# Performance work log

Hardware: AMD Instinct MI355X
Metric: run time of the kernel (lower is better)

## Reference

```python
import jax, jax.numpy as jnp
import numpy as np

MARGIN = 0.2  # init kwarg
_EPS = 1e-12


def _pairwise_dist(x):
    # Euclidean cdist via the Gram trick; safe sqrt so grads stay finite at d=0.
    sq = jnp.sum(x * x, axis=1)
    d2 = sq[:, None] + sq[None, :] - 2.0 * (x @ x.T)
    d2 = jnp.maximum(d2, 0.0)
    safe = jnp.where(d2 > _EPS, d2, _EPS)
    return jnp.where(d2 > _EPS, jnp.sqrt(safe), 0.0)


def setup_inputs() -> dict:
    key = jax.random.key(0)
    k1, k2 = jax.random.split(key)
    B, D = 8192, 128
    embeddings = jax.random.normal(k1, (B, D), dtype=jnp.float32)
    labels = jax.random.randint(k2, (B,), 0, 64)
    return {"embeddings": embeddings, "labels": labels}


def reference(embeddings, labels):
    B = embeddings.shape[0]
    d = _pairwise_dist(embeddings)                      # [B, B]
    eq = labels[None, :] == labels[:, None]             # [B, B] bool (incl. diag)
    pos_mask = eq.astype(d.dtype) - jnp.eye(B, dtype=d.dtype)  # positives, no self
    hardest_positive = jnp.max(d * pos_mask, axis=1)    # [B]
    max_dist = jnp.max(d)
    # push non-negatives (same label, incl. self) out of the min
    hardest_negative = jnp.min(d + max_dist * eq.astype(d.dtype), axis=1)  # [B]
    losses = jax.nn.relu(hardest_positive - hardest_negative + MARGIN)
    return jnp.mean(losses)
```

## Files before the change

kernel.cpp:

```cpp
#include <hip/hip_runtime.h>
#include <hip/hip_bf16.h>


#define BB 8192
#define DD 128
#define MARGIN 0.2f
#define EPS 1e-12f

#define COLS_PER_BLOCK 512
#define STAGE_COLS 64
#define NSTAGES (COLS_PER_BLOCK / STAGE_COLS)
#define STAGE_SHORTS (STAGE_COLS * DD)

typedef __attribute__((ext_vector_type(8))) short short8;
typedef __attribute__((ext_vector_type(4))) float f32x4;

__device__ inline unsigned short f2bf(float f) {
    __hip_bfloat16 h = __float2bfloat16(f);
    unsigned short u;
    __builtin_memcpy(&u, &h, 2);
    return u;
}

__global__ __launch_bounds__(256) void prep_kernel(
    const float* __restrict__ x, const int* __restrict__ lab,
    unsigned short* __restrict__ xb, float2* __restrict__ meta,
    unsigned* __restrict__ hp2, unsigned* __restrict__ mn2) {
    int t = blockIdx.x * blockDim.x + threadIdx.x;
    int row = t >> 5;
    const float4 v = reinterpret_cast<const float4*>(x)[t];

    union { unsigned short u[4]; uint2 w; } p;
    p.u[0] = f2bf(v.x); p.u[1] = f2bf(v.y);
    p.u[2] = f2bf(v.z); p.u[3] = f2bf(v.w);
    reinterpret_cast<uint2*>(xb)[t] = p.w;

    float s = v.x * v.x + v.y * v.y + v.z * v.z + v.w * v.w;
    #pragma unroll
    for (int m = 16; m >= 1; m >>= 1) s += __shfl_xor(s, m, 64);
    if ((t & 31) == 0) meta[row] = make_float2(s, __int_as_float(lab[row]));

    if (t < BB) { hp2[t] = 0u; mn2[t] = 0x7f800000u; }
}

__global__ __launch_bounds__(512, 4) void triplet_main(
    const unsigned short* __restrict__ xb, const float2* __restrict__ meta,
    unsigned* __restrict__ hp2, unsigned* __restrict__ mn2) {
    const int tid  = threadIdx.x;
    const int wave = tid >> 6;
    const int lane = tid & 63;
    const int l15  = lane & 15;
    const int lhi  = lane >> 4;
    const int rbase = blockIdx.x * 128 + wave * 16;
    const int cbase = blockIdx.y * COLS_PER_BLOCK;

    __shared__ unsigned short sb[2][STAGE_SHORTS];
    __shared__ float2 smeta[COLS_PER_BLOCK];

    short8 a[4];
    {
        const unsigned short* ar = xb + (size_t)(rbase + l15) * DD + lhi * 8;
        #pragma unroll
        for (int s = 0; s < 4; ++s)
            a[s] = *reinterpret_cast<const short8*>(ar + s * 32);
    }
    float sqi[4]; int li[4]; float hp[4], mn[4];
    #pragma unroll
    for (int r = 0; r < 4; ++r) {
        float2 mt = meta[rbase + lhi * 4 + r];
        sqi[r] = mt.x; li[r] = __float_as_int(mt.y);
        hp[r] = 0.0f; mn[r] = __builtin_inff();
    }

    smeta[tid] = meta[cbase + tid];

    auto stage = [&](int g, int buf) {
        const char* src_base = (const char*)(xb + (size_t)(cbase + g * STAGE_COLS) * DD);
        #pragma unroll
        for (int r2 = 0; r2 < 2; ++r2) {
            const int o   = r2 * 8192 + tid * 16;
            const int row = o >> 8;
            const int byt = (o & 255) ^ ((row & 7) << 4);
            const char* src = src_base + row * 256 + byt;
            unsigned short* dst = &sb[buf][(r2 * 8192 + wave * 1024) >> 1];
            __builtin_amdgcn_global_load_lds(
                (const __attribute__((address_space(1))) void*)src,
                (__attribute__((address_space(3))) void*)dst, 16, 0, 0);
        }
    };

    const int pread = l15 * 256 + ((lhi * 16) ^ ((l15 & 7) << 4));

    auto compute_stage = [&](int g, int buf) {
        const char* base = (const char*)&sb[buf][0];
        #pragma unroll
        for (int sub = 0; sub < 4; ++sub) {
            short8 b[4];
            #pragma unroll
            for (int ss = 0; ss < 4; ++ss)
                b[ss] = *reinterpret_cast<const short8*>(
                    base + sub * 4096 + (pread ^ (ss << 6)));
            f32x4 acc = {0.0f, 0.0f, 0.0f, 0.0f};
            #pragma unroll
            for (int ss = 0; ss < 4; ++ss)
                acc = __builtin_amdgcn_mfma_f32_16x16x32_bf16(a[ss], b[ss], acc, 0, 0, 0);
            const float2 mj = smeta[g * STAGE_COLS + sub * 16 + l15];
            const float sqj = mj.x;
            const int   lj  = __float_as_int(mj.y);
            #pragma unroll
            for (int r = 0; r < 4; ++r) {
                const float d2 = fmaf(acc[r], -2.0f, sqi[r] + sqj);
                const bool eq = (li[r] == lj);
                hp[r] = fmaxf(hp[r], eq ? d2 : 0.0f);
                mn[r] = fminf(mn[r], eq ? __builtin_inff() : d2);
            }
        }
    };

    stage(0, 0);
    asm volatile("s_waitcnt vmcnt(0)" ::: "memory");
    __syncthreads();
    for (int s = 0; s < NSTAGES; ++s) {
        if (s + 1 < NSTAGES) stage(s + 1, (s + 1) & 1);
        compute_stage(s, s & 1);
        asm volatile("s_waitcnt vmcnt(0)" ::: "memory");
        __syncthreads();
    }

    #pragma unroll
    for (int m = 1; m < 16; m <<= 1) {
        #pragma unroll
        for (int r = 0; r < 4; ++r) {
            hp[r] = fmaxf(hp[r], __shfl_xor(hp[r], m, 64));
            mn[r] = fminf(mn[r], __shfl_xor(mn[r], m, 64));
        }
    }
    if (l15 == 0) {
        #pragma unroll
        for (int r = 0; r < 4; ++r) {
            const int i = rbase + lhi * 4 + r;
            atomicMax(&hp2[i], __float_as_uint(hp[r]));
            atomicMin(&mn2[i], __float_as_uint(mn[r]));
        }
    }
}

__device__ inline float d_of(float d2) {
    return (d2 > EPS) ? sqrtf(d2) : 0.0f;
}

__global__ __launch_bounds__(1024) void finalize_kernel(
    const uint4* __restrict__ hp2v, const uint4* __restrict__ mn2v,
    float* __restrict__ out) {
    float acc = 0.0f;
    #pragma unroll
    for (int it = 0; it < 2; ++it) {
        const int i = it * 1024 + threadIdx.x;
        const uint4 h = hp2v[i];
        const uint4 m = mn2v[i];
        const unsigned hu[4] = {h.x, h.y, h.z, h.w};
        const unsigned mu[4] = {m.x, m.y, m.z, m.w};
        #pragma unroll
        for (int k = 0; k < 4; ++k) {
            const float hpv = d_of(__uint_as_float(hu[k]));
            const float mnv = d_of(__uint_as_float(mu[k]));
            acc += fmaxf(hpv - mnv + MARGIN, 0.0f);
        }
    }
    #pragma unroll
    for (int m = 1; m < 64; m <<= 1) acc += __shfl_xor(acc, m, 64);
    __shared__ float ws[16];
    const int wave = threadIdx.x >> 6;
    if ((threadIdx.x & 63) == 0) ws[wave] = acc;
    __syncthreads();
    if (threadIdx.x == 0) {
        float s = 0.0f;
        #pragma unroll
        for (int w = 0; w < 16; ++w) s += ws[w];
        out[0] = s / (float)BB;
    }
}

extern "C" void kernel_launch(void* const* d_in, const int* in_sizes, int n_in,
                              void* d_out, int out_size, void* d_ws, size_t ws_size,
                              hipStream_t stream) {
    const float* x = (const float*)d_in[0];
    const int* lab = (const int*)d_in[1];
    float* out = (float*)d_out;

    char* ws = (char*)d_ws;
    unsigned short* xb = (unsigned short*)ws;
    float2* meta = (float2*)(ws + (size_t)BB * DD * 2);
    unsigned* hp2 = (unsigned*)(ws + (size_t)BB * DD * 2 + BB * 8);
    unsigned* mn2 = (unsigned*)(ws + (size_t)BB * DD * 2 + BB * 12);

    prep_kernel<<<(BB * DD / 4) / 256, 256, 0, stream>>>(x, lab, xb, meta, hp2, mn2);
    dim3 grid(BB / 128, BB / COLS_PER_BLOCK);
    triplet_main<<<grid, 512, 0, stream>>>(xb, meta, hp2, mn2);
    finalize_kernel<<<1, 1024, 0, stream>>>((const uint4*)hp2, (const uint4*)mn2, out);
}
```

Before: 42.82 us.

## Switch to 32x32x16 MFMA tiles with 4 waves and hoist row norm out of loop

Each wave now computes a 32x32 tile with mfma_32x32x16_bf16 instead of 16x16 tiles, so the block runs 256 threads that each own 32 rows. This increases register reuse of the A fragment and cuts LDS reads per FLOP. The row squared-norm term is pulled out of the inner loop and added once after the max/min reductions, which removes an add per element. The epilogue reductions and atomics now cover 16 accumulators per lane, and the larger register footprint lowers occupancy.

```diff
diff --git a/kernel.cpp b/kernel.cpp
--- a/kernel.cpp
+++ b/kernel.cpp
@@ -8,12 +8,13 @@
 #define EPS 1e-12f
 
 #define COLS_PER_BLOCK 512
+#define ROWS_PER_BLOCK 128
 #define STAGE_COLS 64
 #define NSTAGES (COLS_PER_BLOCK / STAGE_COLS)
 #define STAGE_SHORTS (STAGE_COLS * DD)
 
 typedef __attribute__((ext_vector_type(8))) short short8;
-typedef __attribute__((ext_vector_type(4))) float f32x4;
+typedef __attribute__((ext_vector_type(16))) float f32x16;
 
 __device__ inline unsigned short f2bf(float f) {
     __hip_bfloat16 h = __float2bfloat16(f);
@@ -43,102 +44,108 @@
     if (t < BB) { hp2[t] = 0u; mn2[t] = 0x7f800000u; }
 }
 
-__global__ __launch_bounds__(512, 4) void triplet_main(
+__global__ __launch_bounds__(256, 3) void triplet_main(
     const unsigned short* __restrict__ xb, const float2* __restrict__ meta,
     unsigned* __restrict__ hp2, unsigned* __restrict__ mn2) {
     const int tid  = threadIdx.x;
     const int wave = tid >> 6;
     const int lane = tid & 63;
-    const int l15  = lane & 15;
-    const int lhi  = lane >> 4;
-    const int rbase = blockIdx.x * 128 + wave * 16;
+    const int l31  = lane & 31;
+    const int lh1  = lane >> 5;
+    const int rbase = blockIdx.x * ROWS_PER_BLOCK + wave * 32;
     const int cbase = blockIdx.y * COLS_PER_BLOCK;
 
     __shared__ unsigned short sb[2][STAGE_SHORTS];
     __shared__ float2 smeta[COLS_PER_BLOCK];
 
-    short8 a[4];
+    short8 a[8];
     {
-        const unsigned short* ar = xb + (size_t)(rbase + l15) * DD + lhi * 8;
-        #pragma unroll
-        for (int s = 0; s < 4; ++s)
-            a[s] = *reinterpret_cast<const short8*>(ar + s * 32);
-    }
-    float sqi[4]; int li[4]; float hp[4], mn[4];
-    #pragma unroll
-    for (int r = 0; r < 4; ++r) {
-        float2 mt = meta[rbase + lhi * 4 + r];
-        sqi[r] = mt.x; li[r] = __float_as_int(mt.y);
-        hp[r] = 0.0f; mn[r] = __builtin_inff();
+        const unsigned short* ar = xb + (size_t)(rbase + l31) * DD + lh1 * 8;
+        #pragma unroll
+        for (int s = 0; s < 8; ++s)
+            a[s] = *reinterpret_cast<const short8*>(ar + s * 16);
+    }
+
+    int li[16]; float hp[16], mn[16];
+    #pragma unroll
+    for (int r = 0; r < 16; ++r) {
+        const int rl = (r & 3) + 8 * (r >> 2) + 4 * lh1;
+        li[r] = __float_as_int(meta[rbase + rl].y);
+        hp[r] = -__builtin_inff(); mn[r] = __builtin_inff();
     }
 
     smeta[tid] = meta[cbase + tid];
+    smeta[tid + 256] = meta[cbase + tid + 256];
 
     auto stage = [&](int g, int buf) {
         const char* src_base = (const char*)(xb + (size_t)(cbase + g * STAGE_COLS) * DD);
         #pragma unroll
-        for (int r2 = 0; r2 < 2; ++r2) {
-            const int o   = r2 * 8192 + tid * 16;
+        for (int p = 0; p < 4; ++p) {
+            const int o   = p * 4096 + tid * 16;
             const int row = o >> 8;
             const int byt = (o & 255) ^ ((row & 7) << 4);
             const char* src = src_base + row * 256 + byt;
-            unsigned short* dst = &sb[buf][(r2 * 8192 + wave * 1024) >> 1];
+            char* dst = (char*)&sb[buf][0] + p * 4096 + wave * 1024;
             __builtin_amdgcn_global_load_lds(
                 (const __attribute__((address_space(1))) void*)src,
                 (__attribute__((address_space(3))) void*)dst, 16, 0, 0);
         }
     };
 
-    const int pread = l15 * 256 + ((lhi * 16) ^ ((l15 & 7) << 4));
-
-    auto compute_stage = [&](int g, int buf) {
+    auto compute_group = [&](int st, int gg, int buf) {
         const char* base = (const char*)&sb[buf][0];
-        #pragma unroll
-        for (int sub = 0; sub < 4; ++sub) {
-            short8 b[4];
-            #pragma unroll
-            for (int ss = 0; ss < 4; ++ss)
-                b[ss] = *reinterpret_cast<const short8*>(
-                    base + sub * 4096 + (pread ^ (ss << 6)));
-            f32x4 acc = {0.0f, 0.0f, 0.0f, 0.0f};
-            #pragma unroll
-            for (int ss = 0; ss < 4; ++ss)
-                acc = __builtin_amdgcn_mfma_f32_16x16x32_bf16(a[ss], b[ss], acc, 0, 0, 0);
-            const float2 mj = smeta[g * STAGE_COLS + sub * 16 + l15];
-            const float sqj = mj.x;
-            const int   lj  = __float_as_int(mj.y);
-            #pragma unroll
-            for (int r = 0; r < 4; ++r) {
-                const float d2 = fmaf(acc[r], -2.0f, sqi[r] + sqj);
-                const bool eq = (li[r] == lj);
-                hp[r] = fmaxf(hp[r], eq ? d2 : 0.0f);
-                mn[r] = fminf(mn[r], eq ? __builtin_inff() : d2);
-            }
+        const int jl = gg * 32 + l31;
+        short8 b[8];
+        #pragma unroll
+        for (int s = 0; s < 8; ++s)
+            b[s] = *reinterpret_cast<const short8*>(
+                base + jl * 256 + ((s * 32 + lh1 * 16) ^ ((jl & 7) << 4)));
+        f32x16 acc = {};
+        #pragma unroll
+        for (int s = 0; s < 8; ++s)
+            acc = __builtin_amdgcn_mfma_f32_32x32x16_bf16(a[s], b[s], acc, 0, 0, 0);
+        const float2 mj = smeta[st * STAGE_COLS + jl];
+        const float sqj = mj.x;
+        const int   lj  = __float_as_int(mj.y);
+        #pragma unroll
+        for (int r = 0; r < 16; ++r) {
+            const float d2p = fmaf(acc[r], -2.0f, sqj);
+            const bool eq = (li[r] == lj);
+            hp[r] = fmaxf(hp[r], eq ? d2p : -__builtin_inff());
+            mn[r] = fminf(mn[r], eq ? __builtin_inff() : d2p);
         }
     };
 
     stage(0, 0);
     asm volatile("s_waitcnt vmcnt(0)" ::: "memory");
     __syncthreads();
-    for (int s = 0; s < NSTAGES; ++s) {
-        if (s + 1 < NSTAGES) stage(s + 1, (s + 1) & 1);
-        compute_stage(s, s & 1);
+    for (int st = 0; st < NSTAGES; ++st) {
+        if (st + 1 < NSTAGES) stage(st + 1, (st + 1) & 1);
+        compute_group(st, 0, st & 1);
+        compute_group(st, 1, st & 1);
         asm volatile("s_waitcnt vmcnt(0)" ::: "memory");
         __syncthreads();
     }
 
     #pragma unroll
-    for (int m = 1; m < 16; m <<= 1) {
-        #pragma unroll
-        for (int r = 0; r < 4; ++r) {
+    for (int r = 0; r < 16; ++r) {
+        const int rl = (r & 3) + 8 * (r >> 2) + 4 * lh1;
+        const float sqi = meta[rbase + rl].x;
+        hp[r] = fmaxf(sqi + hp[r], 0.0f);
+        mn[r] = sqi + mn[r];
+    }
+    #pragma unroll
+    for (int m = 1; m < 32; m <<= 1) {
+        #pragma unroll
+        for (int r = 0; r < 16; ++r) {
             hp[r] = fmaxf(hp[r], __shfl_xor(hp[r], m, 64));
             mn[r] = fminf(mn[r], __shfl_xor(mn[r], m, 64));
         }
     }
-    if (l15 == 0) {
-        #pragma unroll
-        for (int r = 0; r < 4; ++r) {
-            const int i = rbase + lhi * 4 + r;
+    if (l31 == 0) {
+        #pragma unroll
+        for (int r = 0; r < 16; ++r) {
+            const int i = rbase + (r & 3) + 8 * (r >> 2) + 4 * lh1;
             atomicMax(&hp2[i], __float_as_uint(hp[r]));
             atomicMin(&mn2[i], __float_as_uint(mn[r]));
         }
@@ -195,7 +202,7 @@
     unsigned* mn2 = (unsigned*)(ws + (size_t)BB * DD * 2 + BB * 12);
 
     prep_kernel<<<(BB * DD / 4) / 256, 256, 0, stream>>>(x, lab, xb, meta, hp2, mn2);
-    dim3 grid(BB / 128, BB / COLS_PER_BLOCK);
-    triplet_main<<<grid, 512, 0, stream>>>(xb, meta, hp2, mn2);
+    dim3 grid(BB / ROWS_PER_BLOCK, BB / COLS_PER_BLOCK);
+    triplet_main<<<grid, 256, 0, stream>>>(xb, meta, hp2, mn2);
     finalize_kernel<<<1, 1024, 0, stream>>>((const uint4*)hp2, (const uint4*)mn2, out);
 }
```

New measurement: 47.57 us. 11.1% more time.
